# Optimization experiments

Hardware: AMD Instinct MI355X
Metric: run time of the kernel (lower is better)

The kernel has to match this reference:

```python
import jax, jax.numpy as jnp
import numpy as np

GRID_SIZE = 5


def kan_layer(x, spline_weight, spline_scaler, grid):
    # x: (B, In); spline_weight: (Out, In, G); spline_scaler: (Out, In); grid: (G,)
    xn = jnp.tanh(x)                                   # (B, In)
    # distances: (B, Out, In, G) via broadcast of (B,1,In,1) against (G,)
    distances = jnp.abs(xn[:, None, :, None] - grid)
    weights = jnp.exp(-distances * spline_scaler[None, :, :, None])
    # double sum over grid then in_features, fused into one einsum
    return jnp.einsum('boig,oig->bo', weights, spline_weight)


def setup_inputs() -> dict:
    key = jax.random.key(0)
    ks = jax.random.split(key, 7)
    B, D_IN, D_H, D_OUT = 2048, 128, 256, 64
    return {
        'x':  jax.random.normal(ks[0], (B, D_IN), dtype=jnp.float32),
        'w1': jax.random.normal(ks[1], (D_H, D_IN, GRID_SIZE), dtype=jnp.float32),
        's1': jax.random.normal(ks[2], (D_H, D_IN), dtype=jnp.float32),
        'w2': jax.random.normal(ks[3], (D_H // 2, D_H, GRID_SIZE), dtype=jnp.float32),
        's2': jax.random.normal(ks[4], (D_H // 2, D_H), dtype=jnp.float32),
        'w3': jax.random.normal(ks[5], (D_OUT, D_H // 2, GRID_SIZE), dtype=jnp.float32),
        's3': jax.random.normal(ks[6], (D_OUT, D_H // 2), dtype=jnp.float32),
    }


def reference(x, w1, s1, w2, s2, w3, s3):
    grid = jnp.linspace(-1.0, 1.0, GRID_SIZE, dtype=jnp.float32)  # registered buffer
    h1 = jax.nn.relu(kan_layer(x, w1, s1, grid))
    h2 = jax.nn.relu(kan_layer(h1, w2, s2, grid))
    out = jax.nn.sigmoid(kan_layer(h2, w3, s3, grid))
    return out
```

## Files before the change

kernel.cpp:

```cpp
#include <hip/hip_runtime.h>
#include <math.h>

#define GRID_N 5
#define LOG2E 1.4426950408889634f
#define EXP2F __builtin_amdgcn_exp2f

__global__ void prep_tab(const float* __restrict__ w, const float* __restrict__ s,
                         float* __restrict__ T, float* __restrict__ Kt, int O, int I) {
    int idx = blockIdx.x * 256 + threadIdx.x;
    if (idx >= O * I) return;
    int o = idx / I, i = idx % I;
    float K = -s[idx] * LOG2E;
    const float gv[5] = {-1.f, -0.5f, 0.f, 0.5f, 1.f};
    float A[6], B[6];
    A[0] = 0.f; B[5] = 0.f;
#pragma unroll
    for (int g = 0; g < 5; g++) {
        float wv = w[idx * GRID_N + g];
        A[g + 1] = A[g] + wv * EXP2F(-K * gv[g]);
    }
#pragma unroll
    for (int g = 4; g >= 0; g--) {
        float wv = w[idx * GRID_N + g];
        B[g] = B[g + 1] + wv * EXP2F(K * gv[g]);
    }
#pragma unroll
    for (int k = 0; k < 6; k++) {
        T[((i * 6 + k) * O + o) * 2 + 0] = A[k];
        T[((i * 6 + k) * O + o) * 2 + 1] = B[k];
    }
    Kt[i * O + o] = K;
}

template<int IN, int OUT, int ACT, int BPT>
__global__ __launch_bounds__(256) void kan_layer(
    const float* __restrict__ xin,
    const float* __restrict__ T,
    const float* __restrict__ Kt,
    float* __restrict__ out)
{
    constexpr int OCH = OUT / 64;
    constexpr int CH  = IN / 64;
    const int lane = threadIdx.x & 63;
    const int wid  = (blockIdx.x << 2) | (threadIdx.x >> 6);
    const int oc   = wid % OCH;
    const int bg   = wid / OCH;
    const int o    = (oc << 6) | lane;
    const int b0   = bg * BPT;

    float xv[BPT][CH];
    int   bo[BPT][CH];
#pragma unroll
    for (int j = 0; j < BPT; j++)
#pragma unroll
        for (int c = 0; c < CH; c++) {
            float v  = xin[(b0 + j) * IN + (c << 6) + lane];
            float ex = EXP2F(2.0f * LOG2E * v);
            float t  = 1.0f - 2.0f / (ex + 1.0f);
            xv[j][c] = t;
            int k = (int)((t + 1.0f) * 2.0f) + 1;
            bo[j][c] = (k > 5 ? 5 : k) * (OUT * 8);
        }

    float acc[BPT];
#pragma unroll
    for (int j = 0; j < BPT; j++) acc[j] = 0.f;

    const char*  Tb = (const char*)T;
    const float* Kp = Kt + o;

#pragma unroll
    for (int c = 0; c < CH; c++) {
#pragma unroll 8
        for (int l = 0; l < 64; l++) {
            const int i = (c << 6) + l;
            float K = Kp[i * OUT];
            const char* Ti = Tb + (size_t)i * (6 * OUT * 8) + (o << 3);
#pragma unroll
            for (int j = 0; j < BPT; j++) {
                float xs = __int_as_float(__builtin_amdgcn_readlane(__float_as_int(xv[j][c]), l));
                int   bs = __builtin_amdgcn_readlane(bo[j][c], l);
                const float2 ab = *(const float2*)(Ti + bs);
                float t = K * xs;
                acc[j] += ab.x * EXP2F(t) + ab.y * EXP2F(-t);
            }
        }
    }

#pragma unroll
    for (int j = 0; j < BPT; j++) {
        float z = acc[j];
        if (ACT == 0) {
            z = fmaxf(z, 0.f);
        } else {
            z = 1.0f / (1.0f + EXP2F(-LOG2E * z));
        }
        out[(b0 + j) * OUT + o] = z;
    }
}

extern "C" void kernel_launch(void* const* d_in, const int* in_sizes, int n_in,
                              void* d_out, int out_size, void* d_ws, size_t ws_size,
                              hipStream_t stream) {
    const float* x  = (const float*)d_in[0];
    const float* w1 = (const float*)d_in[1];
    const float* s1 = (const float*)d_in[2];
    const float* w2 = (const float*)d_in[3];
    const float* s2 = (const float*)d_in[4];
    const float* w3 = (const float*)d_in[5];
    const float* s3 = (const float*)d_in[6];
    float* out = (float*)d_out;

    float* ws  = (float*)d_ws;
    float* h1  = ws;
    float* h2  = h1  + 524288;
    float* T1  = h2  + 262144;
    float* K1  = T1  + 393216;
    float* T2  = K1  + 32768;
    float* K2  = T2  + 393216;
    float* T3  = K2  + 32768;
    float* K3  = T3  + 98304;

    prep_tab<<<128, 256, 0, stream>>>(w1, s1, T1, K1, 256, 128);
    prep_tab<<<128, 256, 0, stream>>>(w2, s2, T2, K2, 128, 256);
    prep_tab<<< 32, 256, 0, stream>>>(w3, s3, T3, K3,  64, 128);

    kan_layer<128, 256, 0, 2><<<1024, 256, 0, stream>>>(x,  T1, K1, h1);
    kan_layer<256, 128, 0, 1><<<1024, 256, 0, stream>>>(h1, T2, K2, h2);
    kan_layer<128,  64, 1, 1><<< 512, 256, 0, stream>>>(h2, T3, K3, out);
}
```

Before: 109.7 us.

## Merge table-prep launches, reorder wave mapping, precompute table offsets, raise layer-2 batch per thread

```diff
diff --git a/kernel.cpp b/kernel.cpp
--- a/kernel.cpp
+++ b/kernel.cpp
@@ -5,25 +5,21 @@
 #define LOG2E 1.4426950408889634f
 #define EXP2F __builtin_amdgcn_exp2f
 
-__global__ void prep_tab(const float* __restrict__ w, const float* __restrict__ s,
-                         float* __restrict__ T, float* __restrict__ Kt, int O, int I) {
-    int idx = blockIdx.x * 256 + threadIdx.x;
-    if (idx >= O * I) return;
+__device__ __forceinline__ void prep_one(const float* __restrict__ w,
+                                         const float* __restrict__ s,
+                                         float* __restrict__ T, float* __restrict__ Kt,
+                                         int O, int I, int idx) {
     int o = idx / I, i = idx % I;
     float K = -s[idx] * LOG2E;
     const float gv[5] = {-1.f, -0.5f, 0.f, 0.5f, 1.f};
     float A[6], B[6];
     A[0] = 0.f; B[5] = 0.f;
 #pragma unroll
-    for (int g = 0; g < 5; g++) {
-        float wv = w[idx * GRID_N + g];
-        A[g + 1] = A[g] + wv * EXP2F(-K * gv[g]);
-    }
+    for (int g = 0; g < 5; g++)
+        A[g + 1] = A[g] + w[idx * GRID_N + g] * EXP2F(-K * gv[g]);
 #pragma unroll
-    for (int g = 4; g >= 0; g--) {
-        float wv = w[idx * GRID_N + g];
-        B[g] = B[g + 1] + wv * EXP2F(K * gv[g]);
-    }
+    for (int g = 4; g >= 0; g--)
+        B[g] = B[g + 1] + w[idx * GRID_N + g] * EXP2F(K * gv[g]);
 #pragma unroll
     for (int k = 0; k < 6; k++) {
         T[((i * 6 + k) * O + o) * 2 + 0] = A[k];
@@ -32,42 +28,56 @@
     Kt[i * O + o] = K;
 }
 
+__global__ __launch_bounds__(256) void prep_all(
+    const float* __restrict__ w1, const float* __restrict__ s1, float* T1, float* K1,
+    const float* __restrict__ w2, const float* __restrict__ s2, float* T2, float* K2,
+    const float* __restrict__ w3, const float* __restrict__ s3, float* T3, float* K3) {
+    int idx = blockIdx.x * 256 + threadIdx.x;
+    if (idx < 32768)       prep_one(w1, s1, T1, K1, 256, 128, idx);
+    else if (idx < 65536)  prep_one(w2, s2, T2, K2, 128, 256, idx - 32768);
+    else if (idx < 73728)  prep_one(w3, s3, T3, K3,  64, 128, idx - 65536);
+}
+
 template<int IN, int OUT, int ACT, int BPT>
 __global__ __launch_bounds__(256) void kan_layer(
     const float* __restrict__ xin,
-    const float* __restrict__ T,
+    const char*  __restrict__ Tb,
     const float* __restrict__ Kt,
     float* __restrict__ out)
 {
-    constexpr int OCH = OUT / 64;
     constexpr int CH  = IN / 64;
+    constexpr int NBG = 2048 / BPT;
+    constexpr unsigned ROWB = OUT * 8;
+
     const int lane = threadIdx.x & 63;
     const int wid  = (blockIdx.x << 2) | (threadIdx.x >> 6);
-    const int oc   = wid % OCH;
-    const int bg   = wid / OCH;
+    const int oc   = wid / NBG;
+    const int bg   = wid % NBG;
     const int o    = (oc << 6) | lane;
     const int b0   = bg * BPT;
 
-    float xv[BPT][CH];
-    int   bo[BPT][CH];
+    float    xv[BPT][CH];
+    unsigned off[BPT][CH];
 #pragma unroll
     for (int j = 0; j < BPT; j++)
 #pragma unroll
         for (int c = 0; c < CH; c++) {
-            float v  = xin[(b0 + j) * IN + (c << 6) + lane];
+            int   i  = (c << 6) + lane;
+            float v  = xin[(b0 + j) * IN + i];
             float ex = EXP2F(2.0f * LOG2E * v);
             float t  = 1.0f - 2.0f / (ex + 1.0f);
             xv[j][c] = t;
             int k = (int)((t + 1.0f) * 2.0f) + 1;
-            bo[j][c] = (k > 5 ? 5 : k) * (OUT * 8);
+            k = k > 5 ? 5 : k;
+            off[j][c] = (unsigned)(i * 6 + k) * ROWB;
         }
 
     float acc[BPT];
 #pragma unroll
     for (int j = 0; j < BPT; j++) acc[j] = 0.f;
 
-    const char*  Tb = (const char*)T;
-    const float* Kp = Kt + o;
+    const unsigned o8 = (unsigned)o * 8u;
+    const float*   Kp = Kt + o;
 
 #pragma unroll
     for (int c = 0; c < CH; c++) {
@@ -75,12 +85,11 @@
         for (int l = 0; l < 64; l++) {
             const int i = (c << 6) + l;
             float K = Kp[i * OUT];
-            const char* Ti = Tb + (size_t)i * (6 * OUT * 8) + (o << 3);
 #pragma unroll
             for (int j = 0; j < BPT; j++) {
-                float xs = __int_as_float(__builtin_amdgcn_readlane(__float_as_int(xv[j][c]), l));
-                int   bs = __builtin_amdgcn_readlane(bo[j][c], l);
-                const float2 ab = *(const float2*)(Ti + bs);
+                float    xs = __int_as_float(__builtin_amdgcn_readlane(__float_as_int(xv[j][c]), l));
+                unsigned os = (unsigned)__builtin_amdgcn_readlane((int)off[j][c], l);
+                const float2 ab = *(const float2*)(Tb + (os + o8));
                 float t = K * xs;
                 acc[j] += ab.x * EXP2F(t) + ab.y * EXP2F(-t);
             }
@@ -90,11 +99,8 @@
 #pragma unroll
     for (int j = 0; j < BPT; j++) {
         float z = acc[j];
-        if (ACT == 0) {
-            z = fmaxf(z, 0.f);
-        } else {
-            z = 1.0f / (1.0f + EXP2F(-LOG2E * z));
-        }
+        if (ACT == 0) z = fmaxf(z, 0.f);
+        else          z = 1.0f / (1.0f + EXP2F(-LOG2E * z));
         out[(b0 + j) * OUT + o] = z;
     }
 }
@@ -121,11 +127,9 @@
     float* T3  = K2  + 32768;
     float* K3  = T3  + 98304;
 
-    prep_tab<<<128, 256, 0, stream>>>(w1, s1, T1, K1, 256, 128);
-    prep_tab<<<128, 256, 0, stream>>>(w2, s2, T2, K2, 128, 256);
-    prep_tab<<< 32, 256, 0, stream>>>(w3, s3, T3, K3,  64, 128);
+    prep_all<<<288, 256, 0, stream>>>(w1, s1, T1, K1, w2, s2, T2, K2, w3, s3, T3, K3);
 
-    kan_layer<128, 256, 0, 2><<<1024, 256, 0, stream>>>(x,  T1, K1, h1);
-    kan_layer<256, 128, 0, 1><<<1024, 256, 0, stream>>>(h1, T2, K2, h2);
-    kan_layer<128,  64, 1, 1><<< 512, 256, 0, stream>>>(h2, T3, K3, out);
+    kan_layer<128, 256, 0, 2><<<1024, 256, 0, stream>>>(x,  (const char*)T1, K1, h1);
+    kan_layer<256, 128, 0, 2><<< 512, 256, 0, stream>>>(h1, (const char*)T2, K2, h2);
+    kan_layer<128,  64, 1, 1><<< 512, 256, 0, stream>>>(h2, (const char*)T3, K3, out);
 }
```

Measured after the change: 123.4 us. 1.12x slower.
